# Performance work log

Hardware: AMD Instinct MI355X
Metric: run time of the kernel (lower is better)

The kernel has to match this reference:

```python
import jax, jax.numpy as jnp
import numpy as np

N = 16384      # number of points (pixels)
C = 64         # value channels of U
D_REF = 5      # bilateral reference feature dim (xy + rgb)


def setup_inputs() -> dict:
    key = jax.random.key(0)
    k1, k2 = jax.random.split(key)
    U = jax.random.normal(k1, (N, C), dtype=jnp.float32)
    ref = jax.random.normal(k2, (N, D_REF), dtype=jnp.float32)
    return {"U": U, "ref": ref}


def reference(U, ref):
    # Gaussian filtering on reference features (exact form of the LSH-approx filter):
    #   out[i] = sum_j exp(-0.5 * ||ref_i - ref_j||^2) * U[j]  -  U[i]
    sq = jnp.sum(ref * ref, axis=-1)                      # [N]
    d2 = sq[:, None] + sq[None, :] - 2.0 * (ref @ ref.T)  # [N, N] squared distances
    K = jnp.exp(-0.5 * jnp.maximum(d2, 0.0))              # [N, N] Gaussian kernel
    return K @ U - U                                       # [N, C]
```

## Files before the change

### kernel.cpp

```cpp
#include <hip/hip_runtime.h>
#include <hip/hip_bf16.h>
#include <stdint.h>

#define N_PTS 16384
#define C_CH  64
#define D_REF 5
#define LOG2E 1.44269504088896340736f
#define IBLOCKS 64

typedef __attribute__((ext_vector_type(8))) short bf16x8;
typedef __attribute__((ext_vector_type(4))) float f32x4;

__device__ __forceinline__ unsigned short bf16rn(float v) {
    unsigned u = __builtin_bit_cast(unsigned, v) + 0x8000u;
    return (unsigned short)(u >> 16);
}
__device__ __forceinline__ float bf16tof(unsigned x) {
    return __builtin_bit_cast(float, x << 16);
}
__device__ __forceinline__ unsigned pack2bf16(float lo, float hi) {
    unsigned a = __builtin_bit_cast(unsigned, lo) + 0x8000u;
    unsigned b = __builtin_bit_cast(unsigned, hi) + 0x8000u;
    return __builtin_amdgcn_perm(b, a, 0x07060302u);
}
__device__ __forceinline__ unsigned cvt2(float lo, float hi) {
#if __has_builtin(__builtin_amdgcn_cvt_pk_bf16_f32)
    typedef __attribute__((ext_vector_type(2))) __bf16 bf162_t;
    bf162_t r = __builtin_amdgcn_cvt_pk_bf16_f32(lo, hi);
    return __builtin_bit_cast(unsigned, r);
#else
    return pack2bf16(lo, hi);
#endif
}
__device__ __forceinline__ float fast_exp2(float x) {
#if __has_builtin(__builtin_amdgcn_exp2f)
    return __builtin_amdgcn_exp2f(x);
#else
    return exp2f(x);
#endif
}
__device__ __forceinline__ void dma16(const unsigned short* g, unsigned short* l) {
#if __has_builtin(__builtin_amdgcn_global_load_lds)
    __builtin_amdgcn_global_load_lds(
        (const __attribute__((address_space(1))) unsigned int*)g,
        (__attribute__((address_space(3))) unsigned int*)l, 16, 0, 0);
#else
    const int lane = threadIdx.x & 63;
    *(uint4*)(l + lane * 8) = *(const uint4*)(g);
#endif
}

__global__ __launch_bounds__(256) void prep_all(
    const float* __restrict__ U, const float* __restrict__ ref,
    unsigned short* __restrict__ packA, unsigned short* __restrict__ packB,
    unsigned short* __restrict__ utPack)
{
    __shared__ unsigned short tile[64 * 80];
    const int bid = blockIdx.x;
    const int t   = threadIdx.x;

    if (bid < 512) {
        const int gid  = bid * 256 + t;
        const int half = gid >> 16;
        const int id   = gid & 0xFFFF;
        const int tile16 = id >> 6;
        const int lane = id & 63;
        const int q    = lane >> 4;
        const int m    = lane & 15;
        const int p = half ? (tile16 * 16 + m)
                           : ((tile16 >> 1) * 32 + (m >> 2) * 8 + (m & 3) + (tile16 & 1) * 4);

        const float* r = ref + (size_t)p * D_REF;
        float rv[5];
        float sq = 0.f;
#pragma unroll
        for (int d = 0; d < 5; ++d) { rv[d] = r[d]; sq += rv[d] * rv[d]; }
        const float h = -0.5f * LOG2E * sq;

        unsigned short bh[5], bl[5];
#pragma unroll
        for (int d = 0; d < 5; ++d) {
            const float base = half ? rv[d] * LOG2E : rv[d];
            bh[d] = bf16rn(base);
            bl[d] = bf16rn(base - bf16tof((unsigned)bh[d]));
        }
        const unsigned short hh  = bf16rn(h);
        const unsigned short hl  = bf16rn(h - bf16tof((unsigned)hh));
        const unsigned short one = 0x3F80;

        unsigned short outv[8];
#pragma unroll
        for (int tt = 0; tt < 8; ++tt) {
            const int k = q * 8 + tt;
            unsigned short v = 0;
            if (!half) {
                if      (k < 5)   v = bh[k];
                else if (k < 10)  v = bh[k - 5];
                else if (k < 15)  v = bl[k - 10];
                else if (k == 15) v = hh;
                else if (k == 16) v = hl;
                else if (k <= 18) v = one;
            } else {
                if      (k < 5)   v = bh[k];
                else if (k < 10)  v = bl[k - 5];
                else if (k < 15)  v = bh[k - 10];
                else if (k <= 16) v = one;
                else if (k == 17) v = hh;
                else if (k == 18) v = hl;
            }
            outv[tt] = v;
        }
        unsigned short* dst = (half ? packB : packA) + ((size_t)tile16 * 64 + lane) * 8;
        *(uint4*)dst = *(uint4*)outv;
    } else {
        const int b  = bid - 512;
        const int j0 = b * 64;
        const int c  = t & 63;
        const int jb = t >> 6;
#pragma unroll
        for (int k = 0; k < 16; ++k) {
            const int jr = jb + k * 4;
            tile[c * 80 + jr] = bf16rn(U[(size_t)(j0 + jr) * C_CH + c]);
        }
        __syncthreads();
#pragma unroll
        for (int rep = 0; rep < 2; ++rep) {
            const int id   = rep * 256 + t;
            const int lane = id & 63;
            const int ct   = (id >> 6) & 3;
            const int kt   = id >> 8;
            const int m    = lane & 15;
            const int q    = lane >> 4;
            const uint4 frag = *(const uint4*)&tile[(ct * 16 + m) * 80 + kt * 32 + q * 8];
            const int jtile  = b * 2 + kt;
            *(uint4*)&utPack[(((size_t)jtile * 4 + ct) * 64 + lane) * 8] = frag;
        }
    }
}

template<int JS>
__global__ __launch_bounds__(256, 4) void lsh_main(
    const float* __restrict__ U,
    const unsigned short* __restrict__ packA,
    const unsigned short* __restrict__ packB,
    const unsigned short* __restrict__ utPack,
    unsigned short* __restrict__ part,
    float* __restrict__ out,
    int use_part)
{
    constexpr int CHUNKS = (N_PTS / JS) / 128;
    __shared__ __align__(16) unsigned short sh[12288];

    const int t    = threadIdx.x;
    const int lane = t & 63;
    const int wave = t >> 6;
    const int q    = lane >> 4;
    const int m    = lane & 15;

    const int ib = blockIdx.x / JS;
    const int js = blockIdx.x % JS;

    bf16x8 bfrag[4];
#pragma unroll
    for (int s = 0; s < 4; ++s) {
        const int itile = ib * 16 + wave * 4 + s;
        bfrag[s] = *(const bf16x8*)(packB + ((size_t)itile * 64 + lane) * 8);
    }

    f32x4 acc[4][4];
#pragma unroll
    for (int s = 0; s < 4; ++s)
#pragma unroll
        for (int ct = 0; ct < 4; ++ct) acc[s][ct] = (f32x4){0.f, 0.f, 0.f, 0.f};

    for (int chunk = 0; chunk < CHUNKS; ++chunk) {
        const unsigned short* srcU = utPack + (size_t)(js * CHUNKS + chunk) * 8192;
        const unsigned short* srcA = packA  + (size_t)(js * CHUNKS + chunk) * 4096;
        __syncthreads();
#pragma unroll
        for (int r = 0; r < 4; ++r)
            dma16(srcU + r * 2048 + wave * 512 + lane * 8, sh + r * 2048 + wave * 512);
#pragma unroll
        for (int r = 0; r < 2; ++r)
            dma16(srcA + r * 2048 + wave * 512 + lane * 8, sh + 8192 + r * 2048 + wave * 512);
        __syncthreads();

#pragma unroll
        for (int kt = 0; kt < 4; ++kt) {
            const bf16x8 ga0 = *(const bf16x8*)(sh + 8192 + (kt * 2 + 0) * 512 + lane * 8);
            const bf16x8 ga1 = *(const bf16x8*)(sh + 8192 + (kt * 2 + 1) * 512 + lane * 8);

            const f32x4 z = (f32x4){0.f, 0.f, 0.f, 0.f};
            bf16x8 sfrag[4];
#pragma unroll
            for (int s = 0; s < 4; ++s) {
                const f32x4 g0 = __builtin_amdgcn_mfma_f32_16x16x32_bf16(ga0, bfrag[s], z, 0, 0, 0);
                const f32x4 g1 = __builtin_amdgcn_mfma_f32_16x16x32_bf16(ga1, bfrag[s], z, 0, 0, 0);
                union { unsigned u[4]; bf16x8 v; } sb;
                sb.u[0] = cvt2(fast_exp2(g0[0]), fast_exp2(g0[1]));
                sb.u[1] = cvt2(fast_exp2(g0[2]), fast_exp2(g0[3]));
                sb.u[2] = cvt2(fast_exp2(g1[0]), fast_exp2(g1[1]));
                sb.u[3] = cvt2(fast_exp2(g1[2]), fast_exp2(g1[3]));
                sfrag[s] = sb.v;
            }
#pragma unroll
            for (int ct = 0; ct < 4; ++ct) {
                const bf16x8 uf = *(const bf16x8*)(sh + kt * 2048 + ct * 512 + lane * 8);
#pragma unroll
                for (int s = 0; s < 4; ++s)
                    acc[s][ct] = __builtin_amdgcn_mfma_f32_16x16x32_bf16(
                        uf, sfrag[s], acc[s][ct], 0, 0, 0);
            }
        }
    }

    if (use_part) {
        unsigned short* dst = part + ((size_t)ib * JS + js) * 16384;
#pragma unroll
        for (int s = 0; s < 4; ++s)
#pragma unroll
            for (int cp = 0; cp < 2; ++cp) {
                uint4 w;
                w.x = cvt2(acc[s][cp*2+0][0], acc[s][cp*2+0][1]);
                w.y = cvt2(acc[s][cp*2+0][2], acc[s][cp*2+0][3]);
                w.z = cvt2(acc[s][cp*2+1][0], acc[s][cp*2+1][1]);
                w.w = cvt2(acc[s][cp*2+1][2], acc[s][cp*2+1][3]);
                *(uint4*)(dst + ((s * 2 + cp) * 256 + t) * 8) = w;
            }
    } else {
#pragma unroll
        for (int s = 0; s < 4; ++s) {
            const int i_glob = ib * 256 + (wave * 4 + s) * 16 + m;
#pragma unroll
            for (int ct = 0; ct < 4; ++ct)
#pragma unroll
                for (int r2 = 0; r2 < 4; ++r2) {
                    const int c = ct * 16 + q * 4 + r2;
                    float val = acc[s][ct][r2];
                    if (js == 0) val -= U[(size_t)i_glob * C_CH + c];
                    atomicAdd(&out[(size_t)i_glob * C_CH + c], val);
                }
        }
    }
}

template<int JS>
__global__ __launch_bounds__(256) void reduce_part(
    const unsigned short* __restrict__ part, const float* __restrict__ U,
    float* __restrict__ out)
{
    const int ib   = blockIdx.x >> 3;
    const int s2cp = blockIdx.x & 7;
    const int tt   = threadIdx.x;
    const int s  = s2cp >> 1, cp = s2cp & 1;
    const int wv = tt >> 6, ln = tt & 63, q = ln >> 4, m = ln & 15;
    const int i  = ib * 256 + (wv * 4 + s) * 16 + m;

    float sums[8];
#pragma unroll
    for (int e = 0; e < 8; ++e) sums[e] = 0.f;

    const unsigned short* base =
        part + (size_t)ib * JS * 16384 + (size_t)(s2cp * 256 + tt) * 8;
#pragma unroll
    for (int js = 0; js < JS; ++js) {
        const uint4 w = *(const uint4*)(base + (size_t)js * 16384);
        sums[0] += bf16tof(w.x & 0xFFFFu); sums[1] += bf16tof(w.x >> 16);
        sums[2] += bf16tof(w.y & 0xFFFFu); sums[3] += bf16tof(w.y >> 16);
        sums[4] += bf16tof(w.z & 0xFFFFu); sums[5] += bf16tof(w.z >> 16);
        sums[6] += bf16tof(w.w & 0xFFFFu); sums[7] += bf16tof(w.w >> 16);
    }

#pragma unroll
    for (int cti = 0; cti < 2; ++cti) {
        const int c0 = (cp * 2 + cti) * 16 + q * 4;
        const f32x4 u = *(const f32x4*)(U + (size_t)i * 64 + c0);
        f32x4 r;
        r[0] = sums[cti * 4 + 0] - u[0];
        r[1] = sums[cti * 4 + 1] - u[1];
        r[2] = sums[cti * 4 + 2] - u[2];
        r[3] = sums[cti * 4 + 3] - u[3];
        *(f32x4*)(out + (size_t)i * 64 + c0) = r;
    }
}

extern "C" void kernel_launch(void* const* d_in, const int* in_sizes, int n_in,
                              void* d_out, int out_size, void* d_ws, size_t ws_size,
                              hipStream_t stream) {
    const float* U   = (const float*)d_in[0];
    const float* ref = (const float*)d_in[1];
    float* out = (float*)d_out;

    unsigned short* utPack = (unsigned short*)d_ws;
    unsigned short* packA  = (unsigned short*)((char*)d_ws + (size_t)2 * 1024 * 1024);
    unsigned short* packB  = (unsigned short*)((char*)d_ws + (size_t)3 * 1024 * 1024);
    unsigned short* part   = (unsigned short*)((char*)d_ws + (size_t)4 * 1024 * 1024);

    const size_t MB = 1024 * 1024;
    prep_all<<<768, 256, 0, stream>>>(U, ref, packA, packB, utPack);

    if (ws_size >= 36 * MB) {
        lsh_main<16><<<IBLOCKS * 16, 256, 0, stream>>>(U, packA, packB, utPack,
                                                       part, out, 1);
        reduce_part<16><<<512, 256, 0, stream>>>(part, U, out);
    } else {
        hipMemsetAsync(d_out, 0, (size_t)out_size * sizeof(float), stream);
        lsh_main<8><<<IBLOCKS * 8, 256, 0, stream>>>(U, packA, packB, utPack,
                                                     part, out, 0);
    }
}
```

Baseline: 116.5 us.

## Double-buffer LDS chunks with async prefetch of next U/A tiles

Splits each j-chunk in half (64 points) and double-buffers the shared memory tiles, issuing the direct-to-LDS loads for the next chunk before computing on the current one and waiting with explicit vmcnt counts. This is meant to overlap global memory latency with the MFMA/exp work instead of stalling at two syncthreads per chunk. It adds manual s_waitcnt/s_barrier handling, which is fragile if the compiler reorders other vector memory ops, and doubles the number of barriers per unit of work.

```diff
diff --git a/kernel.cpp b/kernel.cpp
--- a/kernel.cpp
+++ b/kernel.cpp
@@ -148,8 +148,8 @@
     float* __restrict__ out,
     int use_part)
 {
-    constexpr int CHUNKS = (N_PTS / JS) / 128;
-    __shared__ __align__(16) unsigned short sh[12288];
+    constexpr int CHUNKS = (N_PTS / JS) / 64;
+    __shared__ __align__(16) unsigned short sh[2][6144];
 
     const int t    = threadIdx.x;
     const int lane = t & 63;
@@ -173,22 +173,35 @@
 #pragma unroll
         for (int ct = 0; ct < 4; ++ct) acc[s][ct] = (f32x4){0.f, 0.f, 0.f, 0.f};
 
+    {
+        const unsigned short* srcU = utPack + (size_t)(js * CHUNKS) * 4096;
+        const unsigned short* srcA = packA  + (size_t)(js * CHUNKS) * 2048;
+        dma16(srcU + wave * 512 + lane * 8,        &sh[0][0] + wave * 512);
+        dma16(srcU + 2048 + wave * 512 + lane * 8, &sh[0][0] + 2048 + wave * 512);
+        dma16(srcA + wave * 512 + lane * 8,        &sh[0][4096] + wave * 512);
+    }
+
     for (int chunk = 0; chunk < CHUNKS; ++chunk) {
-        const unsigned short* srcU = utPack + (size_t)(js * CHUNKS + chunk) * 8192;
-        const unsigned short* srcA = packA  + (size_t)(js * CHUNKS + chunk) * 4096;
-        __syncthreads();
-#pragma unroll
-        for (int r = 0; r < 4; ++r)
-            dma16(srcU + r * 2048 + wave * 512 + lane * 8, sh + r * 2048 + wave * 512);
-#pragma unroll
-        for (int r = 0; r < 2; ++r)
-            dma16(srcA + r * 2048 + wave * 512 + lane * 8, sh + 8192 + r * 2048 + wave * 512);
-        __syncthreads();
-
-#pragma unroll
-        for (int kt = 0; kt < 4; ++kt) {
-            const bf16x8 ga0 = *(const bf16x8*)(sh + 8192 + (kt * 2 + 0) * 512 + lane * 8);
-            const bf16x8 ga1 = *(const bf16x8*)(sh + 8192 + (kt * 2 + 1) * 512 + lane * 8);
+        const int cur = chunk & 1;
+        __builtin_amdgcn_s_barrier();
+        if (chunk + 1 < CHUNKS) {
+            const unsigned short* srcU = utPack + (size_t)(js * CHUNKS + chunk + 1) * 4096;
+            const unsigned short* srcA = packA  + (size_t)(js * CHUNKS + chunk + 1) * 2048;
+            unsigned short* dst = &sh[cur ^ 1][0];
+            dma16(srcU + wave * 512 + lane * 8,        dst + wave * 512);
+            dma16(srcU + 2048 + wave * 512 + lane * 8, dst + 2048 + wave * 512);
+            dma16(srcA + wave * 512 + lane * 8,        dst + 4096 + wave * 512);
+            asm volatile("s_waitcnt vmcnt(3)" ::: "memory");
+        } else {
+            asm volatile("s_waitcnt vmcnt(0)" ::: "memory");
+        }
+        __builtin_amdgcn_s_barrier();
+
+        const unsigned short* buf = &sh[cur][0];
+#pragma unroll
+        for (int kt = 0; kt < 2; ++kt) {
+            const bf16x8 ga0 = *(const bf16x8*)(buf + 4096 + kt * 1024 + lane * 8);
+            const bf16x8 ga1 = *(const bf16x8*)(buf + 4096 + kt * 1024 + 512 + lane * 8);
 
             const f32x4 z = (f32x4){0.f, 0.f, 0.f, 0.f};
             bf16x8 sfrag[4];
@@ -205,7 +218,7 @@
             }
 #pragma unroll
             for (int ct = 0; ct < 4; ++ct) {
-                const bf16x8 uf = *(const bf16x8*)(sh + kt * 2048 + ct * 512 + lane * 8);
+                const bf16x8 uf = *(const bf16x8*)(buf + kt * 2048 + ct * 512 + lane * 8);
 #pragma unroll
                 for (int s = 0; s < 4; ++s)
                     acc[s][ct] = __builtin_amdgcn_mfma_f32_16x16x32_bf16(
```

Result: no change. 115.4 us (-1.0%).
